# Kernel tuning notes

Measured on AMD Instinct MI355X. Metric: run time of the kernel, lower is better.

Reference implementation:

```python
import jax, jax.numpy as jnp
import numpy as np

EPS = 0.1

def _kernels():
    # torch: sobel = [[-0.5,0,0.5]]*3 (2D), repeated along depth -> [1,1,3,3,3]
    s = np.array([[-0.5, 0.0, 0.5]] * 3, dtype=np.float32)        # grad along W
    kx = np.tile(s[None, :, :], (3, 1, 1))                        # [3,3,3]
    ky = np.tile(s.T[None, :, :], (3, 1, 1))                      # grad along H
    kz = np.zeros((3, 3, 3), dtype=np.float32)
    kz[0, :, :] = -0.5
    kz[2, :, :] = 0.5                                             # grad along D
    # OIDHW, O=I=1 (channel=1 depthwise)
    return (jnp.asarray(kx)[None, None], jnp.asarray(ky)[None, None], jnp.asarray(kz)[None, None])

KX, KY, KZ = _kernels()

def _conv(x, k):
    return jax.lax.conv_general_dilated(
        x, k, window_strides=(1, 1, 1), padding='VALID',
        dimension_numbers=('NCDHW', 'OIDHW', 'NCDHW'))

def _grads(x):
    # ReplicationPad3d(1) == edge padding on D,H,W
    xp = jnp.pad(x, ((0, 0), (0, 0), (1, 1), (1, 1), (1, 1)), mode='edge')
    return _conv(xp, KX), _conv(xp, KY), _conv(xp, KZ)

def setup_inputs() -> dict:
    key = jax.random.key(0)
    k1, k2, k3 = jax.random.split(key, 3)
    shp = (1, 1, 192, 192, 192)
    return {
        'I': jax.random.normal(k1, shp, dtype=jnp.float32),
        'J': jax.random.normal(k2, shp, dtype=jnp.float32),
        'mask': jax.random.uniform(k3, shp, dtype=jnp.float32),
    }

def reference(I, J, mask):
    Ix, Iy, Iz = _grads(I)
    Jx, Jy, Jz = _grads(J)
    I_mag = Ix * Ix + Iy * Iy + Iz * Iz + EPS * EPS
    J_mag = Jx * Jx + Jy * Jy + Jz * Jz + EPS * EPS
    dot = Ix * Jx + Iy * Jy + Iz * Jz          # == sum over concat channel dim (C=1)
    ngf = (dot * dot) / (I_mag * J_mag)
    return jnp.mean((1.0 - ngf) * mask)
```

## Files before the change

### kernel.cpp

```cpp
#include <hip/hip_runtime.h>

#define NN 192
#define YCHUNK 4
#define BX 48
#define BZ 8

__device__ __forceinline__ void load_row(const float* __restrict__ row,
                                         int x0, int xm, int xp, float v[6]) {
    const float4 c = *reinterpret_cast<const float4*>(row + x0);
    v[1] = c.x; v[2] = c.y; v[3] = c.z; v[4] = c.w;
    v[0] = row[xm];
    v[5] = row[xp];
}

__device__ __forceinline__ void load_slot(const float* __restrict__ A,
                                          int bm, int b0, int bp,
                                          int x0, int xm, int xp,
                                          float sa[4], float sb[4], float tb[4]) {
    float vm[6], v0[6], vp[6];
    load_row(A + bm, x0, xm, xp, vm);
    load_row(A + b0, x0, xm, xp, v0);
    load_row(A + bp, x0, xm, xp, vp);
#pragma unroll
    for (int i = 0; i < 4; ++i) {
        const float am = vm[i + 2] - vm[i];
        const float a0 = v0[i + 2] - v0[i];
        const float ap = vp[i + 2] - vp[i];
        const float bmv = vm[i] + vm[i + 1] + vm[i + 2];
        const float b0v = v0[i] + v0[i + 1] + v0[i + 2];
        const float bpv = vp[i] + vp[i + 1] + vp[i + 2];
        sa[i] = am + a0 + ap;
        sb[i] = bmv + b0v + bpv;
        tb[i] = bpv - bmv;
    }
}

__global__ __launch_bounds__(BX * BZ) void ngf_kernel(const float* __restrict__ I,
                                                      const float* __restrict__ J,
                                                      const float* __restrict__ M,
                                                      float* __restrict__ out) {
    const int x0 = threadIdx.x * 4;
    const int z = blockIdx.y * BZ + threadIdx.y;
    const int ybase = blockIdx.x * YCHUNK;

    const int xm = (x0 == 0) ? 0 : (x0 - 1);
    const int xp = (x0 + 4 > NN - 1) ? (NN - 1) : (x0 + 4);

    const int gzm = (z == 0) ? 0 : z - 1;
    const int gzp = (z == NN - 1) ? (NN - 1) : z + 1;
    const int zbm = gzm * NN, zb0 = z * NN, zbp = gzp * NN;

    float saI[3][4], sbI[3][4], tbI[3][4];
    float saJ[3][4], sbJ[3][4], tbJ[3][4];

    {
        const int gy = (ybase == 0) ? 0 : ybase - 1;
        load_slot(I, (zbm + gy) * NN, (zb0 + gy) * NN, (zbp + gy) * NN, x0, xm, xp,
                  saI[0], sbI[0], tbI[0]);
        load_slot(J, (zbm + gy) * NN, (zb0 + gy) * NN, (zbp + gy) * NN, x0, xm, xp,
                  saJ[0], sbJ[0], tbJ[0]);
        load_slot(I, (zbm + ybase) * NN, (zb0 + ybase) * NN, (zbp + ybase) * NN, x0, xm, xp,
                  saI[1], sbI[1], tbI[1]);
        load_slot(J, (zbm + ybase) * NN, (zb0 + ybase) * NN, (zbp + ybase) * NN, x0, xm, xp,
                  saJ[1], sbJ[1], tbJ[1]);
    }

    float acc = 0.0f;
#pragma unroll
    for (int yy = 0; yy < YCHUNK; ++yy) {
        const int y = ybase + yy;
        const int gyp = (y == NN - 1) ? (NN - 1) : y + 1;
        const int s0 = yy % 3, s1 = (yy + 1) % 3, s2 = (yy + 2) % 3;
        const float4 m4 = *reinterpret_cast<const float4*>(M + (zb0 + y) * NN + x0);
        load_slot(I, (zbm + gyp) * NN, (zb0 + gyp) * NN, (zbp + gyp) * NN, x0, xm, xp,
                  saI[s2], sbI[s2], tbI[s2]);
        load_slot(J, (zbm + gyp) * NN, (zb0 + gyp) * NN, (zbp + gyp) * NN, x0, xm, xp,
                  saJ[s2], sbJ[s2], tbJ[s2]);
        const float mm[4] = {m4.x, m4.y, m4.z, m4.w};
#pragma unroll
        for (int i = 0; i < 4; ++i) {
            const float Ix = saI[s0][i] + saI[s1][i] + saI[s2][i];
            const float Iy = sbI[s2][i] - sbI[s0][i];
            const float Iz = tbI[s0][i] + tbI[s1][i] + tbI[s2][i];
            const float Jx = saJ[s0][i] + saJ[s1][i] + saJ[s2][i];
            const float Jy = sbJ[s2][i] - sbJ[s0][i];
            const float Jz = tbJ[s0][i] + tbJ[s1][i] + tbJ[s2][i];
            const float imag = Ix * Ix + Iy * Iy + Iz * Iz + 0.04f;
            const float jmag = Jx * Jx + Jy * Jy + Jz * Jz + 0.04f;
            const float dot = Ix * Jx + Iy * Jy + Iz * Jz;
            const float ngf = (dot * dot) / (imag * jmag);
            acc += (1.0f - ngf) * mm[i];
        }
    }

    acc *= (1.0f / ((float)NN * (float)NN * (float)NN));
#pragma unroll
    for (int off = 32; off > 0; off >>= 1)
        acc += __shfl_down(acc, off, 64);

    __shared__ float red[(BX * BZ) / 64];
    const int flat = threadIdx.y * BX + threadIdx.x;
    if ((flat & 63) == 0) red[flat >> 6] = acc;
    __syncthreads();
    if (flat == 0) {
        float s = 0.0f;
#pragma unroll
        for (int w = 0; w < (BX * BZ) / 64; ++w) s += red[w];
        atomicAdd(out, s);
    }
}

extern "C" void kernel_launch(void* const* d_in, const int* in_sizes, int n_in,
                              void* d_out, int out_size, void* d_ws, size_t ws_size,
                              hipStream_t stream) {
    const float* I = (const float*)d_in[0];
    const float* J = (const float*)d_in[1];
    const float* M = (const float*)d_in[2];
    float* out = (float*)d_out;

    hipMemsetAsync(d_out, 0, sizeof(float), stream);

    dim3 block(BX, BZ);
    dim3 grid(NN / YCHUNK, NN / BZ);
    ngf_kernel<<<grid, block, 0, stream>>>(I, J, M, out);
}
```

Measured before the change: 138.0 us.

## Stage z-halo planes in double-buffered LDS and stream along y with register prefetch

Each thread used to load its three z-neighbour rows straight from global memory, so every input row was fetched about three times across z-threads. Now the block cooperatively loads one y-plane of I and J (BZ+2 z-rows) into double-buffered shared memory, prefetching the next plane into registers while computing the current one. Each block also covers 8 y-rows instead of 4, which cuts the y-halo overhead, and occupancy is hinted via launch_bounds. The cost is about 30 KB of LDS per block, one barrier per plane, and higher register pressure.

```diff
diff --git a/kernel.cpp b/kernel.cpp
--- a/kernel.cpp
+++ b/kernel.cpp
@@ -1,96 +1,136 @@
 #include <hip/hip_runtime.h>
 
 #define NN 192
-#define YCHUNK 4
 #define BX 48
 #define BZ 8
+#define YC 8
+#define ROWS (BZ + 2)
+#define PLANE_F (2 * ROWS * NN)
+#define NTHR (BX * BZ)
 
-__device__ __forceinline__ void load_row(const float* __restrict__ row,
-                                         int x0, int xm, int xp, float v[6]) {
-    const float4 c = *reinterpret_cast<const float4*>(row + x0);
-    v[1] = c.x; v[2] = c.y; v[3] = c.z; v[4] = c.w;
-    v[0] = row[xm];
-    v[5] = row[xp];
-}
-
-__device__ __forceinline__ void load_slot(const float* __restrict__ A,
-                                          int bm, int b0, int bp,
-                                          int x0, int xm, int xp,
-                                          float sa[4], float sb[4], float tb[4]) {
-    float vm[6], v0[6], vp[6];
-    load_row(A + bm, x0, xm, xp, vm);
-    load_row(A + b0, x0, xm, xp, v0);
-    load_row(A + bp, x0, xm, xp, vp);
-#pragma unroll
-    for (int i = 0; i < 4; ++i) {
-        const float am = vm[i + 2] - vm[i];
-        const float a0 = v0[i + 2] - v0[i];
-        const float ap = vp[i + 2] - vp[i];
-        const float bmv = vm[i] + vm[i + 1] + vm[i + 2];
-        const float b0v = v0[i] + v0[i + 1] + v0[i + 2];
-        const float bpv = vp[i] + vp[i + 1] + vp[i + 2];
-        sa[i] = am + a0 + ap;
-        sb[i] = bmv + b0v + bpv;
-        tb[i] = bpv - bmv;
-    }
-}
-
-__global__ __launch_bounds__(BX * BZ) void ngf_kernel(const float* __restrict__ I,
+__global__ __launch_bounds__(NTHR, 3) void ngf_kernel(const float* __restrict__ I,
                                                       const float* __restrict__ J,
                                                       const float* __restrict__ M,
                                                       float* __restrict__ out) {
-    const int x0 = threadIdx.x * 4;
-    const int z = blockIdx.y * BZ + threadIdx.y;
-    const int ybase = blockIdx.x * YCHUNK;
+    __shared__ float lds[2 * PLANE_F];
 
-    const int xm = (x0 == 0) ? 0 : (x0 - 1);
-    const int xp = (x0 + 4 > NN - 1) ? (NN - 1) : (x0 + 4);
+    const int tx = threadIdx.x;
+    const int tz = threadIdx.y;
+    const int flat = tz * BX + tx;
+    const int x0 = tx * 4;
+    const int xm = (tx == 0) ? 0 : (x0 - 1);
+    const int xp = (tx == BX - 1) ? (NN - 1) : (x0 + 4);
+    const int z0 = blockIdx.y * BZ;
+    const int z = z0 + tz;
+    const int ybase = blockIdx.x * YC;
 
-    const int gzm = (z == 0) ? 0 : z - 1;
-    const int gzp = (z == NN - 1) ? (NN - 1) : z + 1;
-    const int zbm = gzm * NN, zb0 = z * NN, zbp = gzp * NN;
+    const float* sp[3];
+    int gi[3];
+    int le[3];
+    {
+        const int eidx[3] = {flat, flat + NTHR, flat + 2 * NTHR};
+#pragma unroll
+        for (int j = 0; j < 3; ++j) {
+            const int e = eidx[j];
+            const int arr = e / (ROWS * BX);
+            const int rem = e - arr * (ROWS * BX);
+            const int zr = rem / BX;
+            const int xg = rem - zr * BX;
+            int zc = z0 - 1 + zr;
+            zc = zc < 0 ? 0 : (zc > NN - 1 ? NN - 1 : zc);
+            sp[j] = arr ? J : I;
+            gi[j] = zc * NN * NN + xg * 4;
+            le[j] = e * 4;
+        }
+    }
+    const bool has3 = (flat < 960 - 2 * NTHR);
 
-    float saI[3][4], sbI[3][4], tbI[3][4];
-    float saJ[3][4], sbJ[3][4], tbJ[3][4];
-
+    float4 r0, r1, r2;
     {
-        const int gy = (ybase == 0) ? 0 : ybase - 1;
-        load_slot(I, (zbm + gy) * NN, (zb0 + gy) * NN, (zbp + gy) * NN, x0, xm, xp,
-                  saI[0], sbI[0], tbI[0]);
-        load_slot(J, (zbm + gy) * NN, (zb0 + gy) * NN, (zbp + gy) * NN, x0, xm, xp,
-                  saJ[0], sbJ[0], tbJ[0]);
-        load_slot(I, (zbm + ybase) * NN, (zb0 + ybase) * NN, (zbp + ybase) * NN, x0, xm, xp,
-                  saI[1], sbI[1], tbI[1]);
-        load_slot(J, (zbm + ybase) * NN, (zb0 + ybase) * NN, (zbp + ybase) * NN, x0, xm, xp,
-                  saJ[1], sbJ[1], tbJ[1]);
+        const int yc = (ybase == 0) ? 0 : (ybase - 1);
+        const int yr = yc * NN;
+        r0 = *(const float4*)(sp[0] + gi[0] + yr);
+        r1 = *(const float4*)(sp[1] + gi[1] + yr);
+        if (has3) r2 = *(const float4*)(sp[2] + gi[2] + yr);
     }
 
+    float sa[2][3][4], sb[2][3][4], tb[2][3][4];
     float acc = 0.0f;
+    float4 m_cur = make_float4(0.f, 0.f, 0.f, 0.f);
+
 #pragma unroll
-    for (int yy = 0; yy < YCHUNK; ++yy) {
-        const int y = ybase + yy;
-        const int gyp = (y == NN - 1) ? (NN - 1) : y + 1;
-        const int s0 = yy % 3, s1 = (yy + 1) % 3, s2 = (yy + 2) % 3;
-        const float4 m4 = *reinterpret_cast<const float4*>(M + (zb0 + y) * NN + x0);
-        load_slot(I, (zbm + gyp) * NN, (zb0 + gyp) * NN, (zbp + gyp) * NN, x0, xm, xp,
-                  saI[s2], sbI[s2], tbI[s2]);
-        load_slot(J, (zbm + gyp) * NN, (zb0 + gyp) * NN, (zbp + gyp) * NN, x0, xm, xp,
-                  saJ[s2], sbJ[s2], tbJ[s2]);
-        const float mm[4] = {m4.x, m4.y, m4.z, m4.w};
+    for (int k = 0; k < YC + 2; ++k) {
+        const int bufF = (k & 1) * PLANE_F;
+
+        *(float4*)&lds[bufF + le[0]] = r0;
+        *(float4*)&lds[bufF + le[1]] = r1;
+        if (has3) *(float4*)&lds[bufF + le[2]] = r2;
+        __syncthreads();
+
+        {
+            int yn = ybase + k;
+            yn = yn > NN - 1 ? NN - 1 : yn;
+            const int yr = yn * NN;
+            r0 = *(const float4*)(sp[0] + gi[0] + yr);
+            r1 = *(const float4*)(sp[1] + gi[1] + yr);
+            if (has3) r2 = *(const float4*)(sp[2] + gi[2] + yr);
+        }
+        float4 m_next;
+        {
+            int my = ybase + k - 1;
+            my = my < 0 ? 0 : (my > NN - 1 ? NN - 1 : my);
+            m_next = *(const float4*)(M + (z * NN + my) * NN + x0);
+        }
+
+        const int s = k % 3;
 #pragma unroll
-        for (int i = 0; i < 4; ++i) {
-            const float Ix = saI[s0][i] + saI[s1][i] + saI[s2][i];
-            const float Iy = sbI[s2][i] - sbI[s0][i];
-            const float Iz = tbI[s0][i] + tbI[s1][i] + tbI[s2][i];
-            const float Jx = saJ[s0][i] + saJ[s1][i] + saJ[s2][i];
-            const float Jy = sbJ[s2][i] - sbJ[s0][i];
-            const float Jz = tbJ[s0][i] + tbJ[s1][i] + tbJ[s2][i];
-            const float imag = Ix * Ix + Iy * Iy + Iz * Iz + 0.04f;
-            const float jmag = Jx * Jx + Jy * Jy + Jz * Jz + 0.04f;
-            const float dot = Ix * Jx + Iy * Jy + Iz * Jz;
-            const float ngf = (dot * dot) / (imag * jmag);
-            acc += (1.0f - ngf) * mm[i];
+        for (int arr = 0; arr < 2; ++arr) {
+            float fa[4] = {0.f, 0.f, 0.f, 0.f};
+            float fb[4] = {0.f, 0.f, 0.f, 0.f};
+            float blo[4], bhi[4];
+#pragma unroll
+            for (int dz = 0; dz < 3; ++dz) {
+                const int rb = bufF + arr * (ROWS * NN) + (tz + dz) * NN;
+                const float4 c = *(const float4*)&lds[rb + x0];
+                const float L = lds[rb + xm];
+                const float R = lds[rb + xp];
+                const float w[6] = {L, c.x, c.y, c.z, c.w, R};
+#pragma unroll
+                for (int i = 0; i < 4; ++i) {
+                    const float a = w[i + 2] - w[i];
+                    const float b = w[i] + w[i + 1] + w[i + 2];
+                    fa[i] += a;
+                    fb[i] += b;
+                    if (dz == 0) blo[i] = b;
+                    if (dz == 2) bhi[i] = b;
+                }
+            }
+#pragma unroll
+            for (int i = 0; i < 4; ++i) {
+                sa[arr][s][i] = fa[i];
+                sb[arr][s][i] = fb[i];
+                tb[arr][s][i] = bhi[i] - blo[i];
+            }
         }
+
+        if (k >= 2) {
+            const int sA = (k - 2) % 3, sB = (k - 1) % 3, sC = k % 3;
+            const float mm[4] = {m_cur.x, m_cur.y, m_cur.z, m_cur.w};
+#pragma unroll
+            for (int i = 0; i < 4; ++i) {
+                const float Ix = sa[0][sA][i] + sa[0][sB][i] + sa[0][sC][i];
+                const float Iy = sb[0][sC][i] - sb[0][sA][i];
+                const float Iz = tb[0][sA][i] + tb[0][sB][i] + tb[0][sC][i];
+                const float Jx = sa[1][sA][i] + sa[1][sB][i] + sa[1][sC][i];
+                const float Jy = sb[1][sC][i] - sb[1][sA][i];
+                const float Jz = tb[1][sA][i] + tb[1][sB][i] + tb[1][sC][i];
+                const float im = Ix * Ix + Iy * Iy + Iz * Iz + 0.04f;
+                const float jm = Jx * Jx + Jy * Jy + Jz * Jz + 0.04f;
+                const float dot = Ix * Jx + Iy * Jy + Iz * Jz;
+                acc += (1.0f - (dot * dot) / (im * jm)) * mm[i];
+            }
+        }
+        m_cur = m_next;
     }
 
     acc *= (1.0f / ((float)NN * (float)NN * (float)NN));
@@ -98,15 +138,14 @@
     for (int off = 32; off > 0; off >>= 1)
         acc += __shfl_down(acc, off, 64);
 
-    __shared__ float red[(BX * BZ) / 64];
-    const int flat = threadIdx.y * BX + threadIdx.x;
+    __shared__ float red[NTHR / 64];
     if ((flat & 63) == 0) red[flat >> 6] = acc;
     __syncthreads();
     if (flat == 0) {
-        float s = 0.0f;
+        float ssum = 0.0f;
 #pragma unroll
-        for (int w = 0; w < (BX * BZ) / 64; ++w) s += red[w];
-        atomicAdd(out, s);
+        for (int w = 0; w < NTHR / 64; ++w) ssum += red[w];
+        atomicAdd(out, ssum);
     }
 }
 
@@ -121,6 +160,6 @@
     hipMemsetAsync(d_out, 0, sizeof(float), stream);
 
     dim3 block(BX, BZ);
-    dim3 grid(NN / YCHUNK, NN / BZ);
+    dim3 grid(NN / YC, NN / BZ);
     ngf_kernel<<<grid, block, 0, stream>>>(I, J, M, out);
 }
```

Measured after the change: 203.8 us. 47.6% more time.

## Software-pipeline row loads with double-buffered raw registers and larger Y chunk

Applied to the files above, without the earlier changes.

Restructures the per-thread Y sweep so the raw loads for the next Y row (all six I/J depth rows plus the mask) are issued into a second register buffer before the current row is folded and reduced, overlapping memory latency with arithmetic. It also changes the block shape to 48x4 threads covering 8 Y rows each, and adds a launch-bounds occupancy hint. The intent is to hide global load latency and amortise the two halo rows over more outputs. The cost is higher register pressure, which may cut occupancy.

```diff
diff --git a/kernel.cpp b/kernel.cpp
--- a/kernel.cpp
+++ b/kernel.cpp
@@ -1,96 +1,121 @@
 #include <hip/hip_runtime.h>
 
 #define NN 192
-#define YCHUNK 4
 #define BX 48
-#define BZ 8
+#define BZ 4
+#define YC 8
+#define NTHR (BX * BZ)
 
-__device__ __forceinline__ void load_row(const float* __restrict__ row,
-                                         int x0, int xm, int xp, float v[6]) {
-    const float4 c = *reinterpret_cast<const float4*>(row + x0);
-    v[1] = c.x; v[2] = c.y; v[3] = c.z; v[4] = c.w;
-    v[0] = row[xm];
-    v[5] = row[xp];
-}
+struct Raw {
+    float4 c[6];
+    float  L[6];
+    float  R[6];
+};
 
-__device__ __forceinline__ void load_slot(const float* __restrict__ A,
-                                          int bm, int b0, int bp,
-                                          int x0, int xm, int xp,
-                                          float sa[4], float sb[4], float tb[4]) {
-    float vm[6], v0[6], vp[6];
-    load_row(A + bm, x0, xm, xp, vm);
-    load_row(A + b0, x0, xm, xp, v0);
-    load_row(A + bp, x0, xm, xp, vp);
+__device__ __forceinline__ void load_plane(const float* const base[6], int yrow,
+                                           int dL, int dR, Raw& r) {
 #pragma unroll
-    for (int i = 0; i < 4; ++i) {
-        const float am = vm[i + 2] - vm[i];
-        const float a0 = v0[i + 2] - v0[i];
-        const float ap = vp[i + 2] - vp[i];
-        const float bmv = vm[i] + vm[i + 1] + vm[i + 2];
-        const float b0v = v0[i] + v0[i + 1] + v0[i + 2];
-        const float bpv = vp[i] + vp[i + 1] + vp[i + 2];
-        sa[i] = am + a0 + ap;
-        sb[i] = bmv + b0v + bpv;
-        tb[i] = bpv - bmv;
+    for (int d = 0; d < 6; ++d) {
+        const float* p = base[d] + yrow;
+        r.c[d] = *reinterpret_cast<const float4*>(p);
+        r.L[d] = p[dL];
+        r.R[d] = p[dR];
     }
 }
 
-__global__ __launch_bounds__(BX * BZ) void ngf_kernel(const float* __restrict__ I,
+__device__ __forceinline__ void fold_rows(const float4& cm, float Lm, float Rm,
+                                          const float4& c0, float L0, float R0,
+                                          const float4& cp, float Lp, float Rp,
+                                          float sa[4], float sb[4], float tb[4]) {
+    const float wm[6] = {Lm, cm.x, cm.y, cm.z, cm.w, Rm};
+    const float w0[6] = {L0, c0.x, c0.y, c0.z, c0.w, R0};
+    const float wp[6] = {Lp, cp.x, cp.y, cp.z, cp.w, Rp};
+#pragma unroll
+    for (int i = 0; i < 4; ++i) {
+        const float am = wm[i + 2] - wm[i];
+        const float a0 = w0[i + 2] - w0[i];
+        const float ap = wp[i + 2] - wp[i];
+        const float bm = wm[i] + wm[i + 1] + wm[i + 2];
+        const float b0 = w0[i] + w0[i + 1] + w0[i + 2];
+        const float bp = wp[i] + wp[i + 1] + wp[i + 2];
+        sa[i] = am + a0 + ap;
+        sb[i] = bm + b0 + bp;
+        tb[i] = bp - bm;
+    }
+}
+
+__global__ __launch_bounds__(NTHR, 2) void ngf_kernel(const float* __restrict__ I,
                                                       const float* __restrict__ J,
                                                       const float* __restrict__ M,
                                                       float* __restrict__ out) {
-    const int x0 = threadIdx.x * 4;
-    const int z = blockIdx.y * BZ + threadIdx.y;
-    const int ybase = blockIdx.x * YCHUNK;
-
-    const int xm = (x0 == 0) ? 0 : (x0 - 1);
-    const int xp = (x0 + 4 > NN - 1) ? (NN - 1) : (x0 + 4);
+    const int tx = threadIdx.x;
+    const int tz = threadIdx.y;
+    const int x0 = tx * 4;
+    const int dL = (tx == 0) ? 0 : -1;
+    const int dR = (tx == BX - 1) ? 3 : 4;
+    const int z = blockIdx.y * BZ + tz;
+    const int ybase = blockIdx.x * YC;
 
     const int gzm = (z == 0) ? 0 : z - 1;
     const int gzp = (z == NN - 1) ? (NN - 1) : z + 1;
-    const int zbm = gzm * NN, zb0 = z * NN, zbp = gzp * NN;
 
-    float saI[3][4], sbI[3][4], tbI[3][4];
-    float saJ[3][4], sbJ[3][4], tbJ[3][4];
+    const float* base[6] = {
+        I + gzm * NN * NN + x0, I + z * NN * NN + x0, I + gzp * NN * NN + x0,
+        J + gzm * NN * NN + x0, J + z * NN * NN + x0, J + gzp * NN * NN + x0};
 
-    {
-        const int gy = (ybase == 0) ? 0 : ybase - 1;
-        load_slot(I, (zbm + gy) * NN, (zb0 + gy) * NN, (zbp + gy) * NN, x0, xm, xp,
-                  saI[0], sbI[0], tbI[0]);
-        load_slot(J, (zbm + gy) * NN, (zb0 + gy) * NN, (zbp + gy) * NN, x0, xm, xp,
-                  saJ[0], sbJ[0], tbJ[0]);
-        load_slot(I, (zbm + ybase) * NN, (zb0 + ybase) * NN, (zbp + ybase) * NN, x0, xm, xp,
-                  saI[1], sbI[1], tbI[1]);
-        load_slot(J, (zbm + ybase) * NN, (zb0 + ybase) * NN, (zbp + ybase) * NN, x0, xm, xp,
-                  saJ[1], sbJ[1], tbJ[1]);
-    }
+    float sa[2][3][4], sb[2][3][4], tb[2][3][4];
+    Raw A, B;
+
+    load_plane(base, ((ybase == 0) ? 0 : (ybase - 1)) * NN, dL, dR, A);
+    load_plane(base, ybase * NN, dL, dR, B);
+    fold_rows(A.c[0], A.L[0], A.R[0], A.c[1], A.L[1], A.R[1], A.c[2], A.L[2], A.R[2],
+              sa[0][0], sb[0][0], tb[0][0]);
+    fold_rows(A.c[3], A.L[3], A.R[3], A.c[4], A.L[4], A.R[4], A.c[5], A.L[5], A.R[5],
+              sa[1][0], sb[1][0], tb[1][0]);
+    fold_rows(B.c[0], B.L[0], B.R[0], B.c[1], B.L[1], B.R[1], B.c[2], B.L[2], B.R[2],
+              sa[0][1], sb[0][1], tb[0][1]);
+    fold_rows(B.c[3], B.L[3], B.R[3], B.c[4], B.L[4], B.R[4], B.c[5], B.L[5], B.R[5],
+              sa[1][1], sb[1][1], tb[1][1]);
+    load_plane(base, (ybase + 1) * NN, dL, dR, A);
+    float4 mcur = *reinterpret_cast<const float4*>(M + (z * NN + ybase) * NN + x0);
 
     float acc = 0.0f;
 #pragma unroll
-    for (int yy = 0; yy < YCHUNK; ++yy) {
-        const int y = ybase + yy;
-        const int gyp = (y == NN - 1) ? (NN - 1) : y + 1;
-        const int s0 = yy % 3, s1 = (yy + 1) % 3, s2 = (yy + 2) % 3;
-        const float4 m4 = *reinterpret_cast<const float4*>(M + (zb0 + y) * NN + x0);
-        load_slot(I, (zbm + gyp) * NN, (zb0 + gyp) * NN, (zbp + gyp) * NN, x0, xm, xp,
-                  saI[s2], sbI[s2], tbI[s2]);
-        load_slot(J, (zbm + gyp) * NN, (zb0 + gyp) * NN, (zbp + gyp) * NN, x0, xm, xp,
-                  saJ[s2], sbJ[s2], tbJ[s2]);
-        const float mm[4] = {m4.x, m4.y, m4.z, m4.w};
+    for (int yy = 0; yy < YC; ++yy) {
+        const int j = yy + 2;
+        Raw& cur = (yy & 1) ? B : A;
+        Raw& nxt = (yy & 1) ? A : B;
+
+        float4 mnxt = mcur;
+        if (yy < YC - 1) {
+            int gy = ybase + yy + 2;
+            gy = (gy > NN - 1) ? (NN - 1) : gy;
+            load_plane(base, gy * NN, dL, dR, nxt);
+            mnxt = *reinterpret_cast<const float4*>(M + (z * NN + (ybase + yy + 1)) * NN + x0);
+        }
+
+        const int sC = j % 3;
+        fold_rows(cur.c[0], cur.L[0], cur.R[0], cur.c[1], cur.L[1], cur.R[1],
+                  cur.c[2], cur.L[2], cur.R[2], sa[0][sC], sb[0][sC], tb[0][sC]);
+        fold_rows(cur.c[3], cur.L[3], cur.R[3], cur.c[4], cur.L[4], cur.R[4],
+                  cur.c[5], cur.L[5], cur.R[5], sa[1][sC], sb[1][sC], tb[1][sC]);
+
+        const int s0 = yy % 3, s1 = (yy + 1) % 3;
+        const float mm[4] = {mcur.x, mcur.y, mcur.z, mcur.w};
 #pragma unroll
         for (int i = 0; i < 4; ++i) {
-            const float Ix = saI[s0][i] + saI[s1][i] + saI[s2][i];
-            const float Iy = sbI[s2][i] - sbI[s0][i];
-            const float Iz = tbI[s0][i] + tbI[s1][i] + tbI[s2][i];
-            const float Jx = saJ[s0][i] + saJ[s1][i] + saJ[s2][i];
-            const float Jy = sbJ[s2][i] - sbJ[s0][i];
-            const float Jz = tbJ[s0][i] + tbJ[s1][i] + tbJ[s2][i];
-            const float imag = Ix * Ix + Iy * Iy + Iz * Iz + 0.04f;
-            const float jmag = Jx * Jx + Jy * Jy + Jz * Jz + 0.04f;
+            const float Ix = sa[0][s0][i] + sa[0][s1][i] + sa[0][sC][i];
+            const float Iy = sb[0][sC][i] - sb[0][s0][i];
+            const float Iz = tb[0][s0][i] + tb[0][s1][i] + tb[0][sC][i];
+            const float Jx = sa[1][s0][i] + sa[1][s1][i] + sa[1][sC][i];
+            const float Jy = sb[1][sC][i] - sb[1][s0][i];
+            const float Jz = tb[1][s0][i] + tb[1][s1][i] + tb[1][sC][i];
+            const float im = Ix * Ix + Iy * Iy + Iz * Iz + 0.04f;
+            const float jm = Jx * Jx + Jy * Jy + Jz * Jz + 0.04f;
             const float dot = Ix * Jx + Iy * Jy + Iz * Jz;
-            const float ngf = (dot * dot) / (imag * jmag);
-            acc += (1.0f - ngf) * mm[i];
+            acc += (1.0f - (dot * dot) / (im * jm)) * mm[i];
         }
+        mcur = mnxt;
     }
 
     acc *= (1.0f / ((float)NN * (float)NN * (float)NN));
@@ -98,14 +123,14 @@
     for (int off = 32; off > 0; off >>= 1)
         acc += __shfl_down(acc, off, 64);
 
-    __shared__ float red[(BX * BZ) / 64];
-    const int flat = threadIdx.y * BX + threadIdx.x;
+    __shared__ float red[NTHR / 64];
+    const int flat = tz * BX + tx;
     if ((flat & 63) == 0) red[flat >> 6] = acc;
     __syncthreads();
     if (flat == 0) {
         float s = 0.0f;
 #pragma unroll
-        for (int w = 0; w < (BX * BZ) / 64; ++w) s += red[w];
+        for (int w = 0; w < NTHR / 64; ++w) s += red[w];
         atomicAdd(out, s);
     }
 }
@@ -121,6 +146,6 @@
     hipMemsetAsync(d_out, 0, sizeof(float), stream);
 
     dim3 block(BX, BZ);
-    dim3 grid(NN / YCHUNK, NN / BZ);
+    dim3 grid(NN / YC, NN / BZ);
     ngf_kernel<<<grid, block, 0, stream>>>(I, J, M, out);
 }
```

Result: faster. 130.3 us (-5.6%).
